# Kernel optimization log

Hardware: AMD Instinct MI355X
Metric: run time of the kernel (lower is better)

Reference implementation:

```python
import jax, jax.numpy as jnp
import numpy as np

N = 32768       # total nodes across the batch of graphs
E = 524288      # total edges
D = 512         # feature dim (dimensions = [512, 512, 512])
G = 512         # number of graphs (64 nodes each)


def setup_inputs() -> dict:
    key = jax.random.key(0)
    ks = jax.random.split(key, 16)
    inp = {
        'feat': jax.random.normal(ks[0], (N, D), jnp.float32),
        'src': jax.random.randint(ks[1], (E,), 0, N, jnp.int32),
        'dst': jax.random.randint(ks[2], (E,), 0, N, jnp.int32),
        'adj_vals': jax.random.uniform(ks[3], (E,), jnp.float32),
        'graph_ids': (jnp.arange(N, dtype=jnp.int32) // (N // G)),
        'W0': jax.random.normal(ks[4], (D, D), jnp.float32) * 0.05,
        'b0': jnp.zeros((D,), jnp.float32),
        'W1': jax.random.normal(ks[5], (D, D), jnp.float32) * 0.05,
        'b1': jnp.zeros((D,), jnp.float32),
        'gW1': jax.random.normal(ks[6], (D, D), jnp.float32) * 0.05,
        'gb1': jnp.zeros((D,), jnp.float32),
        'gW2': jax.random.normal(ks[7], (D, D), jnp.float32) * 0.05,
        'gb2': jnp.zeros((D,), jnp.float32),
        'gW3': jax.random.normal(ks[8], (D, D), jnp.float32) * 0.05,
        'gb3': jnp.zeros((D,), jnp.float32),
        'gWs': jax.random.normal(ks[9], (D, D), jnp.float32) * 0.05,
        'gbs': jnp.zeros((D,), jnp.float32),
    }
    return inp


def reference(feat, src, dst, adj_vals, graph_ids,
              W0, b0, W1, b1,
              gW1, gb1, gW2, gb2, gW3, gb3, gWs, gbs):
    # GCN layer: act(A_hat @ (X W) + b), A_hat given as weighted edge list
    def gcn(h, W, b, act):
        support = h @ W                              # [N, D]
        msg = adj_vals[:, None] * support[src]       # [E, D]
        agg = jax.ops.segment_sum(msg, dst, num_segments=N)
        return act(agg + b)

    h = gcn(feat, W0, b0, jax.nn.relu)               # hidden layer, act=relu
    h = gcn(h, W1, b1, lambda x: x)                  # last layer, identity act

    # pooling: per-graph mean readout -> sigmoid -> repeat-expand back to nodes
    ones = jnp.ones((N, 1), h.dtype)
    counts = jax.ops.segment_sum(ones, graph_ids, num_segments=G)   # [G, 1]
    pooled = jax.ops.segment_sum(h, graph_ids, num_segments=G) / counts
    g = jax.nn.sigmoid(pooled)[graph_ids]            # [N, D] repeat-expanded

    z = jax.nn.relu(g @ gW1 + gb1)
    z = jax.nn.relu(z @ gW2 + gb2)
    z = jax.nn.relu(z @ gW3 + gb3)
    return z + (g @ gWs + gbs)
```

## Files before the change

kernel.cpp:

```cpp
#include <hip/hip_runtime.h>

typedef unsigned int u32;
typedef unsigned short u16;

typedef __attribute__((ext_vector_type(8))) __bf16 bf16x8;
typedef __attribute__((ext_vector_type(4))) float f32x4;
typedef __attribute__((ext_vector_type(2))) float f32x2;
typedef __attribute__((ext_vector_type(4))) u32 u32x4;

#define N_NODES 32768
#define N_EDGES 524288
#define DIM 512
#define N_GRAPHS 512
#define ECAP_ROW 768
#define ECAP 1216
#define ELDS_SZ (ECAP + ECAP / 32 + 1)
#define NB_CONV 8192
#define NB_TR 1536

__device__ __forceinline__ u16 f2b(float f) {
  union { float f; u32 u; } v; v.f = f;
  u32 r = v.u + 0x7FFFu + ((v.u >> 16) & 1u);
  return (u16)(r >> 16);
}
__device__ __forceinline__ u32 pack2(float a, float b) {
  return (u32)f2b(a) | ((u32)f2b(b) << 16);
}
__device__ __forceinline__ float blo(u32 u) { union { u32 u; float f; } v; v.u = u << 16; return v.f; }
__device__ __forceinline__ float bhi(u32 u) { union { u32 u; float f; } v; v.u = u & 0xFFFF0000u; return v.f; }
__device__ __forceinline__ float b2f(u16 u) { union { u32 u; float f; } v; v.u = ((u32)u) << 16; return v.f; }

__device__ __forceinline__ void async16(const void* g, void* l) {
  __builtin_amdgcn_global_load_lds(
      (const __attribute__((address_space(1))) u32*)g,
      (__attribute__((address_space(3))) u32*)l, 16, 0, 0);
}

__device__ __forceinline__ int eidx(int i) { return i + (i >> 5); }

__device__ __forceinline__ void acc8(f32x2* a, u32x4 raw, float v) {
  f32x2 v2 = {v, v};
  a[0] += v2 * f32x2{blo(raw.x), bhi(raw.x)};
  a[1] += v2 * f32x2{blo(raw.y), bhi(raw.y)};
  a[2] += v2 * f32x2{blo(raw.z), bhi(raw.z)};
  a[3] += v2 * f32x2{blo(raw.w), bhi(raw.w)};
}

struct WPack {
  const float* src[6];
  u16* dst[6];
};
__global__ __launch_bounds__(256)
void k_prep(const float* __restrict__ feat, u16* __restrict__ featb, WPack wp,
            const int* __restrict__ dstv, int* __restrict__ counts) {
  __shared__ float tile[32][33];
  const int bid = blockIdx.x, tid = threadIdx.x;
  if (bid < NB_CONV) {
    int i = bid * 256 + tid;
    const float4* p = (const float4*)feat;
    float4 a = p[2 * i], b = p[2 * i + 1];
    uint4 o;
    o.x = pack2(a.x, a.y); o.y = pack2(a.z, a.w);
    o.z = pack2(b.x, b.y); o.w = pack2(b.z, b.w);
    ((uint4*)featb)[i] = o;
  } else if (bid < NB_CONV + NB_TR) {
    int idx = bid - NB_CONV;
    int bz = idx >> 8, rem = idx & 255, by = rem >> 4, bx = rem & 15;
    const float* W = wp.src[bz];
    u16* Wt = wp.dst[bz];
    int tx = tid & 31, ty = tid >> 5;
    int bx32 = bx * 32, by32 = by * 32;
    #pragma unroll
    for (int i = 0; i < 4; i++)
      tile[ty + 8 * i][tx] = W[(size_t)(by32 + ty + 8 * i) * DIM + bx32 + tx];
    __syncthreads();
    #pragma unroll
    for (int i = 0; i < 4; i++)
      Wt[(size_t)(bx32 + ty + 8 * i) * DIM + by32 + tx] = f2b(tile[tx][ty + 8 * i]);
  } else {
    int i = (bid - NB_CONV - NB_TR) * 256 + tid;
    atomicAdd(&counts[dstv[i]], 1);
  }
}

__global__ void k_scan(const int* __restrict__ counts, int* __restrict__ offsets,
                       int* __restrict__ cursor) {
  __shared__ int part[1024];
  int t = threadIdx.x;
  const int4* c4 = (const int4*)counts;
  int4 cv[8];
  #pragma unroll
  for (int j = 0; j < 8; j++) cv[j] = c4[t * 8 + j];
  int loc[32];
  int s = 0;
  #pragma unroll
  for (int j = 0; j < 8; j++) {
    loc[4 * j + 0] = s; s += cv[j].x;
    loc[4 * j + 1] = s; s += cv[j].y;
    loc[4 * j + 2] = s; s += cv[j].z;
    loc[4 * j + 3] = s; s += cv[j].w;
  }
  part[t] = s;
  __syncthreads();
  for (int off = 1; off < 1024; off <<= 1) {
    int v = (t >= off) ? part[t - off] : 0;
    __syncthreads();
    part[t] += v;
    __syncthreads();
  }
  int excl = (t == 0) ? 0 : part[t - 1];
  #pragma unroll
  for (int j = 0; j < 8; j++) {
    int4 o = make_int4(excl + loc[4 * j], excl + loc[4 * j + 1],
                       excl + loc[4 * j + 2], excl + loc[4 * j + 3]);
    ((int4*)offsets)[t * 8 + j] = o;
    ((int4*)cursor)[t * 8 + j] = o;
  }
  if (t == 1023) offsets[N_NODES] = excl + s;
}

__global__ void k_fill(const int* __restrict__ src, const int* __restrict__ dst,
                       const float* __restrict__ vals, int* __restrict__ cursor,
                       int2* __restrict__ epack) {
  int i = blockIdx.x * 256 + threadIdx.x;
  if (i >= N_EDGES) return;
  int d = dst[i];
  int p = atomicAdd(&cursor[d], 1);
  epack[p] = make_int2(src[i] | ((d & 63) << 15), __float_as_int(vals[i]));
}

__global__ __launch_bounds__(256)
void k_gemm_bt(const u16* __restrict__ A, const u16* __restrict__ Bt,
               u16* __restrict__ Cout, int M, int Nout, int K) {
  __shared__ __align__(16) u16 As[128 * 32];
  __shared__ __align__(16) u16 Bs[128 * 32];
  const int tid = threadIdx.x;
  const int l = tid & 63;
  const int w = tid >> 6;
  const int mBase = blockIdx.x * 128;
  const int nBase = blockIdx.y * 128;
  const int wm = (w >> 1) * 64;
  const int wn = (w & 1) * 64;
  const int lrow = l >> 2;
  const int lcol = (l & 3) * 8;
  const int q = l >> 4;
  const int r = l & 15;
  f32x4 acc[4][4] = {};

  for (int k0 = 0; k0 < K; k0 += 32) {
    #pragma unroll
    for (int p = 0; p < 2; p++) {
      int row = w * 32 + p * 16 + lrow;
      async16(A + (size_t)(mBase + row) * K + k0 + lcol, (char*)As + w * 2048 + p * 1024);
      async16(Bt + (size_t)(nBase + row) * K + k0 + lcol, (char*)Bs + w * 2048 + p * 1024);
    }
    __syncthreads();
    bf16x8 af[4], bfr[4];
    #pragma unroll
    for (int i = 0; i < 4; i++) af[i] = *(const bf16x8*)&As[(wm + i * 16 + r) * 32 + q * 8];
    #pragma unroll
    for (int j = 0; j < 4; j++) bfr[j] = *(const bf16x8*)&Bs[(wn + j * 16 + r) * 32 + q * 8];
    #pragma unroll
    for (int i = 0; i < 4; i++)
      #pragma unroll
      for (int j = 0; j < 4; j++)
        acc[i][j] = __builtin_amdgcn_mfma_f32_16x16x32_bf16(af[i], bfr[j], acc[i][j], 0, 0, 0);
    __syncthreads();
  }

  #pragma unroll
  for (int i = 0; i < 4; i++) {
    #pragma unroll
    for (int j = 0; j < 4; j++) {
      int col = nBase + wn + j * 16 + r;
      #pragma unroll
      for (int reg = 0; reg < 4; reg++) {
        int rowg = mBase + wm + i * 16 + q * 4 + reg;
        Cout[(size_t)rowg * Nout + col] = f2b(acc[i][j][reg]);
      }
    }
  }
}

template <bool RELU, bool ADDEND, bool OUTF32, bool SIGMOID>
__global__ __launch_bounds__(256)
void k_gemm_small(const u16* __restrict__ A, const u16* __restrict__ Bt,
                  const float* __restrict__ bias, const u16* __restrict__ addend,
                  void* __restrict__ Cout, int Nout, int K) {
  __shared__ __align__(16) u16 As[64 * 32];
  __shared__ __align__(16) u16 Bs[64 * 32];
  const int tid = threadIdx.x;
  const int l = tid & 63;
  const int w = tid >> 6;
  const int mBase = blockIdx.x * 64;
  const int nBase = blockIdx.y * 64;
  const int wm = (w >> 1) * 32;
  const int wn = (w & 1) * 32;
  const int lrow = tid >> 2;
  const int lcol = (tid & 3) * 8;
  const int q = l >> 4;
  const int r = l & 15;
  f32x4 acc[2][2] = {};

  for (int k0 = 0; k0 < K; k0 += 32) {
    async16(A + (size_t)(mBase + lrow) * K + k0 + lcol, (char*)As + tid * 16);
    async16(Bt + (size_t)(nBase + lrow) * K + k0 + lcol, (char*)Bs + tid * 16);
    __syncthreads();
    bf16x8 af[2], bfr[2];
    #pragma unroll
    for (int i = 0; i < 2; i++) af[i] = *(const bf16x8*)&As[(wm + i * 16 + r) * 32 + q * 8];
    #pragma unroll
    for (int j = 0; j < 2; j++) bfr[j] = *(const bf16x8*)&Bs[(wn + j * 16 + r) * 32 + q * 8];
    #pragma unroll
    for (int i = 0; i < 2; i++)
      #pragma unroll
      for (int j = 0; j < 2; j++)
        acc[i][j] = __builtin_amdgcn_mfma_f32_16x16x32_bf16(af[i], bfr[j], acc[i][j], 0, 0, 0);
    __syncthreads();
  }

  #pragma unroll
  for (int i = 0; i < 2; i++) {
    #pragma unroll
    for (int j = 0; j < 2; j++) {
      int col = nBase + wn + j * 16 + r;
      float bv = bias[col];
      #pragma unroll
      for (int reg = 0; reg < 4; reg++) {
        int rowg = mBase + wm + i * 16 + q * 4 + reg;
        float v = acc[i][j][reg] + bv;
        if (ADDEND) v += b2f(addend[(size_t)rowg * Nout + col]);
        if (RELU) v = fmaxf(v, 0.0f);
        if (SIGMOID) v = 1.0f / (1.0f + expf(-v));
        if (OUTF32) ((float*)Cout)[(size_t)rowg * Nout + col] = v;
        else ((u16*)Cout)[(size_t)rowg * Nout + col] = f2b(v);
      }
    }
  }
}

__global__ __launch_bounds__(256)
void k_agg_row(const u16* __restrict__ support, const int* __restrict__ offsets,
               const int2* __restrict__ epack, const float* __restrict__ bias,
               u16* __restrict__ outp) {
  __shared__ int2 eLds[ECAP_ROW];
  __shared__ unsigned char permLds[32];
  const int tid = threadIdx.x;
  const int chunk = blockIdx.x & 7;
  const int gidx  = blockIdx.x >> 3;
  const int rowBase = gidx * 32;
  const int e0b = offsets[rowBase];
  const int nb = offsets[rowBase + 32] - e0b;
  const bool fits = (nb <= ECAP_ROW);

  if (tid < 32) {
    int deg = offsets[rowBase + tid + 1] - offsets[rowBase + tid];
    u32 key = ((u32)deg << 8) | (u32)tid;
    #pragma unroll
    for (int k = 2; k <= 32; k <<= 1) {
      #pragma unroll
      for (int j = k >> 1; j >= 1; j >>= 1) {
        u32 o = __shfl_xor(key, j);
        bool lower = (tid & j) == 0;
        bool asc = (tid & k) == 0;
        key = ((key < o) == (lower == asc)) ? key : o;
      }
    }
    permLds[tid] = (unsigned char)(key & 255u);
  }
  if (fits) {
    for (int i = tid; i < nb; i += 256) eLds[i] = epack[e0b + i];
  }
  __syncthreads();

  const int wi = tid >> 6;
  const int l  = tid & 63;
  const int grp = l >> 3;
  const int li  = l & 7;
  const int colOff = chunk * 64 + li * 8;
  const u16* spc = support + colOff;

  const int rl = permLds[wi * 8 + grp];
  const int r = rowBase + rl;
  const int re0 = offsets[r] - e0b;
  const int deg = offsets[r + 1] - e0b - re0;

  f32x2 a[4];
  {
    const float4* bp = (const float4*)(bias + colOff);
    float4 x = bp[0], y = bp[1];
    a[0] = f32x2{x.x, x.y}; a[1] = f32x2{x.z, x.w};
    a[2] = f32x2{y.x, y.y}; a[3] = f32x2{y.z, y.w};
  }

  if (fits) {
    int i = 0;
    for (; i + 8 <= deg; i += 8) {
      int2 p[8];
      #pragma unroll
      for (int j = 0; j < 8; j++) p[j] = eLds[re0 + i + j];
      u32x4 rw[8];
      #pragma unroll
      for (int j = 0; j < 8; j++)
        rw[j] = *(const u32x4*)(spc + (size_t)(p[j].x & 32767) * DIM);
      #pragma unroll
      for (int j = 0; j < 8; j++) acc8(a, rw[j], __int_as_float(p[j].y));
    }
    for (; i < deg; i++) {
      int2 p = eLds[re0 + i];
      u32x4 rw = *(const u32x4*)(spc + (size_t)(p.x & 32767) * DIM);
      acc8(a, rw, __int_as_float(p.y));
    }
  } else {
    for (int i = 0; i < deg; i++) {
      int2 p = epack[e0b + re0 + i];
      u32x4 rw = *(const u32x4*)(spc + (size_t)(p.x & 32767) * DIM);
      acc8(a, rw, __int_as_float(p.y));
    }
  }

  #pragma unroll
  for (int i = 0; i < 4; i++) {
    a[i].x = fmaxf(a[i].x, 0.0f);
    a[i].y = fmaxf(a[i].y, 0.0f);
  }
  u32x4 o;
  o.x = pack2(a[0].x, a[0].y); o.y = pack2(a[1].x, a[1].y);
  o.z = pack2(a[2].x, a[2].y); o.w = pack2(a[3].x, a[3].y);
  *(u32x4*)(outp + (size_t)r * DIM + colOff) = o;
}

__global__ __launch_bounds__(256)
void k_agg_pool(const u16* __restrict__ support, const int* __restrict__ offsets,
                const int2* __restrict__ epack, u16* __restrict__ outp) {
  __shared__ int2 eLds[ELDS_SZ];
  __shared__ float redLds[256];

  const int tid = threadIdx.x;
  const int chunk = blockIdx.x & 7;
  const int cidx = blockIdx.x >> 3;
  const int rowBase = cidx * 64;
  const int e0b = offsets[rowBase];
  const int nb = offsets[rowBase + 64] - e0b;
  const bool fits = (nb <= ECAP);

  if (fits) {
    for (int i = tid; i < nb; i += 256) eLds[eidx(i)] = epack[e0b + i];
  }
  __syncthreads();

  const int slot = tid >> 3;
  const int li = tid & 7;
  const int colOff = chunk * 64 + li * 8;
  const u16* spc = support + colOff;
  const int e0 = (nb * slot) >> 5;
  const int e1 = (nb * (slot + 1)) >> 5;

  f32x2 psum[4] = {};

  auto consume = [&](int2 p, u32x4 rw) {
    float v = __int_as_float(p.y);
    f32x2 v2 = {v, v};
    psum[0] += v2 * f32x2{blo(rw.x), bhi(rw.x)};
    psum[1] += v2 * f32x2{blo(rw.y), bhi(rw.y)};
    psum[2] += v2 * f32x2{blo(rw.z), bhi(rw.z)};
    psum[3] += v2 * f32x2{blo(rw.w), bhi(rw.w)};
  };

  if (fits) {
    int i = e0;
    for (; i + 8 <= e1; i += 8) {
      int2 p[8];
      #pragma unroll
      for (int j = 0; j < 8; j++) p[j] = eLds[eidx(i + j)];
      u32x4 rw[8];
      #pragma unroll
      for (int j = 0; j < 8; j++)
        rw[j] = *(const u32x4*)(spc + (size_t)(p[j].x & 32767) * DIM);
      #pragma unroll
      for (int j = 0; j < 8; j++) consume(p[j], rw[j]);
    }
    for (; i < e1; i++) {
      int2 p = eLds[eidx(i)];
      u32x4 rw = *(const u32x4*)(spc + (size_t)(p.x & 32767) * DIM);
      consume(p, rw);
    }
  } else {
    for (int i = e0; i < e1; i++) {
      int2 p = epack[e0b + i];
      u32x4 rw = *(const u32x4*)(spc + (size_t)(p.x & 32767) * DIM);
      consume(p, rw);
    }
  }

  #pragma unroll
  for (int k = 0; k < 4; k++) {
    psum[k].x += __shfl_xor(psum[k].x, 8);  psum[k].y += __shfl_xor(psum[k].y, 8);
    psum[k].x += __shfl_xor(psum[k].x, 16); psum[k].y += __shfl_xor(psum[k].y, 16);
    psum[k].x += __shfl_xor(psum[k].x, 32); psum[k].y += __shfl_xor(psum[k].y, 32);
  }
  const int wi = tid >> 6;
  if (((tid >> 3) & 7) == 0) {
    #pragma unroll
    for (int k = 0; k < 4; k++) {
      redLds[wi * 64 + li * 8 + 2 * k]     = psum[k].x;
      redLds[wi * 64 + li * 8 + 2 * k + 1] = psum[k].y;
    }
  }
  __syncthreads();
  if (tid < 64) {
    float s = redLds[tid] + redLds[64 + tid] + redLds[128 + tid] + redLds[192 + tid];
    outp[(size_t)cidx * DIM + chunk * 64 + tid] = f2b(s * (1.0f / 64.0f));
  }
}

__global__ void k_expand(const float* __restrict__ small, float* __restrict__ out) {
  int i = blockIdx.x * 256 + threadIdx.x;
  int col4 = i & 127;
  int node = i >> 7;
  float4 v = ((const float4*)small)[((node >> 6) << 7) + col4];
  ((float4*)out)[i] = v;
}

extern "C" void kernel_launch(void* const* d_in, const int* in_sizes, int n_in,
                              void* d_out, int out_size, void* d_ws, size_t ws_size,
                              hipStream_t stream) {
  const float* feat = (const float*)d_in[0];
  const int* src    = (const int*)d_in[1];
  const int* dst    = (const int*)d_in[2];
  const float* adj  = (const float*)d_in[3];
  const float* W0  = (const float*)d_in[5];
  const float* b0  = (const float*)d_in[6];
  const float* W1  = (const float*)d_in[7];
  const float* b1  = (const float*)d_in[8];
  const float* gW1 = (const float*)d_in[9];
  const float* gb1 = (const float*)d_in[10];
  const float* gW2 = (const float*)d_in[11];
  const float* gb2 = (const float*)d_in[12];
  const float* gW3 = (const float*)d_in[13];
  const float* gb3 = (const float*)d_in[14];
  const float* gWs = (const float*)d_in[15];
  const float* gbs = (const float*)d_in[16];

  char* ws = (char*)d_ws;
  size_t off = 0;
  auto alloc = [&](size_t bytes) -> void* {
    void* p = ws + off;
    off = (off + bytes + 255) & ~(size_t)255;
    return p;
  };
  u16* bufA = (u16*)alloc((size_t)N_NODES * DIM * 2);
  u16* bufB = (u16*)alloc((size_t)N_NODES * DIM * 2);
  u16* wt[6];
  for (int i = 0; i < 6; i++) wt[i] = (u16*)alloc((size_t)DIM * DIM * 2);
  int* counts   = (int*)alloc((size_t)N_NODES * 4);
  int* offsets  = (int*)alloc((size_t)(N_NODES + 1) * 4);
  int* cursor   = (int*)alloc((size_t)N_NODES * 4);
  int2* epack   = (int2*)alloc((size_t)N_EDGES * 8);
  u16* qb       = (u16*)alloc((size_t)N_GRAPHS * DIM * 2);
  u16* gfeat    = (u16*)alloc((size_t)N_GRAPHS * DIM * 2);
  u16* z1       = (u16*)alloc((size_t)N_GRAPHS * DIM * 2);
  u16* z2       = (u16*)alloc((size_t)N_GRAPHS * DIM * 2);
  u16* z3       = (u16*)alloc((size_t)N_GRAPHS * DIM * 2);
  float* osmall = (float*)alloc((size_t)N_GRAPHS * DIM * 4);

  (void)hipMemsetAsync(counts, 0, (size_t)N_NODES * 4, stream);

  WPack wp;
  wp.src[0] = W0; wp.src[1] = W1; wp.src[2] = gW1; wp.src[3] = gW2; wp.src[4] = gW3; wp.src[5] = gWs;
  for (int i = 0; i < 6; i++) wp.dst[i] = wt[i];

  k_prep<<<NB_CONV + NB_TR + N_EDGES / 256, 256, 0, stream>>>(feat, bufA, wp, dst, counts);
  k_scan<<<1, 1024, 0, stream>>>(counts, offsets, cursor);
  k_fill<<<N_EDGES / 256, 256, 0, stream>>>(src, dst, adj, cursor, epack);

  k_gemm_bt<<<dim3(N_NODES / 128, DIM / 128), 256, 0, stream>>>(bufA, wt[0], bufB, N_NODES, DIM, DIM);
  k_agg_row<<<8192, 256, 0, stream>>>(bufB, offsets, epack, b0, bufA);
  k_agg_pool<<<4096, 256, 0, stream>>>(bufA, offsets, epack, qb);
  k_gemm_small<false, false, false, true><<<dim3(8, 8), 256, 0, stream>>>(qb, wt[1], b1, nullptr, gfeat, DIM, DIM);

  k_gemm_small<true, false, false, false><<<dim3(8, 8), 256, 0, stream>>>(gfeat, wt[2], gb1, nullptr, z1, DIM, DIM);
  k_gemm_small<true, false, false, false><<<dim3(8, 8), 256, 0, stream>>>(z1, wt[3], gb2, nullptr, z2, DIM, DIM);
  k_gemm_small<true, false, false, false><<<dim3(8, 8), 256, 0, stream>>>(z2, wt[4], gb3, nullptr, z3, DIM, DIM);
  k_gemm_small<false, true, true, false><<<dim3(8, 8), 256, 0, stream>>>(gfeat, wt[5], gbs, z3, osmall, DIM, DIM);

  k_expand<<<(N_NODES * DIM / 4) / 256, 256, 0, stream>>>(osmall, (float*)d_out);
}
```

Before: 383.9 us.

## Fuse the five small per-graph GEMMs into one LDS-resident kernel

```diff
diff --git a/kernel.cpp b/kernel.cpp
--- a/kernel.cpp
+++ b/kernel.cpp
@@ -17,6 +17,7 @@
 #define ELDS_SZ (ECAP + ECAP / 32 + 1)
 #define NB_CONV 8192
 #define NB_TR 1536
+#define FFP 520
 
 __device__ __forceinline__ u16 f2b(float f) {
   union { float f; u32 u; } v; v.f = f;
@@ -182,59 +183,87 @@
   }
 }
 
-template <bool RELU, bool ADDEND, bool OUTF32, bool SIGMOID>
-__global__ __launch_bounds__(256)
-void k_gemm_small(const u16* __restrict__ A, const u16* __restrict__ Bt,
-                  const float* __restrict__ bias, const u16* __restrict__ addend,
-                  void* __restrict__ Cout, int Nout, int K) {
-  __shared__ __align__(16) u16 As[64 * 32];
-  __shared__ __align__(16) u16 Bs[64 * 32];
+template <int ACT>
+__device__ __forceinline__ void ff_stage(const u16* Ain, const u16* __restrict__ Wt,
+                                         const float* __restrict__ bias, u16* Aout,
+                                         int l, int wv) {
+  const int r15 = l & 15;
+  const int q = l >> 4;
+  #pragma unroll
+  for (int t = 0; t < 4; t++) {
+    const int ct = wv * 4 + t;
+    f32x4 acc = {};
+    #pragma unroll
+    for (int k0 = 0; k0 < 512; k0 += 32) {
+      bf16x8 af = *(const bf16x8*)&Ain[r15 * FFP + k0 + q * 8];
+      bf16x8 bf = *(const bf16x8*)&Wt[(size_t)(ct * 16 + r15) * 512 + k0 + q * 8];
+      acc = __builtin_amdgcn_mfma_f32_16x16x32_bf16(af, bf, acc, 0, 0, 0);
+    }
+    const int c = ct * 16 + r15;
+    const float bv = bias[c];
+    #pragma unroll
+    for (int reg = 0; reg < 4; reg++) {
+      float v = acc[reg] + bv;
+      v = ACT ? fmaxf(v, 0.0f) : (1.0f / (1.0f + expf(-v)));
+      Aout[(q * 4 + reg) * FFP + c] = f2b(v);
+    }
+  }
+}
+
+__global__ __launch_bounds__(512)
+void k_ff(const u16* __restrict__ qb,
+          const u16* __restrict__ w1, const float* __restrict__ b1,
+          const u16* __restrict__ w2, const float* __restrict__ gb1,
+          const u16* __restrict__ w3, const float* __restrict__ gb2,
+          const u16* __restrict__ w4, const float* __restrict__ gb3,
+          const u16* __restrict__ w5, const float* __restrict__ gbs,
+          float* __restrict__ osmall) {
+  __shared__ __align__(16) u16 G[16 * FFP];
+  __shared__ __align__(16) u16 Z0[16 * FFP];
+  __shared__ __align__(16) u16 Z1[16 * FFP];
   const int tid = threadIdx.x;
   const int l = tid & 63;
-  const int w = tid >> 6;
-  const int mBase = blockIdx.x * 64;
-  const int nBase = blockIdx.y * 64;
-  const int wm = (w >> 1) * 32;
-  const int wn = (w & 1) * 32;
-  const int lrow = tid >> 2;
-  const int lcol = (tid & 3) * 8;
+  const int wv = tid >> 6;
+  const int rBase = blockIdx.x * 16;
+
+  for (int i = tid; i < 16 * 64; i += 512) {
+    int row = i >> 6, c8 = (i & 63) * 8;
+    *(bf16x8*)&Z0[row * FFP + c8] = *(const bf16x8*)&qb[(size_t)(rBase + row) * 512 + c8];
+  }
+  __syncthreads();
+
+  ff_stage<0>(Z0, w1, b1, G, l, wv);
+  __syncthreads();
+  ff_stage<1>(G, w2, gb1, Z0, l, wv);
+  __syncthreads();
+  ff_stage<1>(Z0, w3, gb2, Z1, l, wv);
+  __syncthreads();
+  ff_stage<1>(Z1, w4, gb3, Z0, l, wv);
+  __syncthreads();
+
+  {
+    const int r15 = l & 15;
+    const int q = l >> 6 ? 0 : l >> 4;
+  }
+  const int r15 = l & 15;
   const int q = l >> 4;
-  const int r = l & 15;
-  f32x4 acc[2][2] = {};
-
-  for (int k0 = 0; k0 < K; k0 += 32) {
-    async16(A + (size_t)(mBase + lrow) * K + k0 + lcol, (char*)As + tid * 16);
-    async16(Bt + (size_t)(nBase + lrow) * K + k0 + lcol, (char*)Bs + tid * 16);
-    __syncthreads();
-    bf16x8 af[2], bfr[2];
-    #pragma unroll
-    for (int i = 0; i < 2; i++) af[i] = *(const bf16x8*)&As[(wm + i * 16 + r) * 32 + q * 8];
-    #pragma unroll
-    for (int j = 0; j < 2; j++) bfr[j] = *(const bf16x8*)&Bs[(wn + j * 16 + r) * 32 + q * 8];
-    #pragma unroll
-    for (int i = 0; i < 2; i++)
-      #pragma unroll
-      for (int j = 0; j < 2; j++)
-        acc[i][j] = __builtin_amdgcn_mfma_f32_16x16x32_bf16(af[i], bfr[j], acc[i][j], 0, 0, 0);
-    __syncthreads();
-  }
-
-  #pragma unroll
-  for (int i = 0; i < 2; i++) {
-    #pragma unroll
-    for (int j = 0; j < 2; j++) {
-      int col = nBase + wn + j * 16 + r;
-      float bv = bias[col];
-      #pragma unroll
-      for (int reg = 0; reg < 4; reg++) {
-        int rowg = mBase + wm + i * 16 + q * 4 + reg;
-        float v = acc[i][j][reg] + bv;
-        if (ADDEND) v += b2f(addend[(size_t)rowg * Nout + col]);
-        if (RELU) v = fmaxf(v, 0.0f);
-        if (SIGMOID) v = 1.0f / (1.0f + expf(-v));
-        if (OUTF32) ((float*)Cout)[(size_t)rowg * Nout + col] = v;
-        else ((u16*)Cout)[(size_t)rowg * Nout + col] = f2b(v);
-      }
+  #pragma unroll
+  for (int t = 0; t < 4; t++) {
+    const int ct = wv * 4 + t;
+    f32x4 acc = {};
+    #pragma unroll
+    for (int k0 = 0; k0 < 512; k0 += 32) {
+      bf16x8 af = *(const bf16x8*)&G[r15 * FFP + k0 + q * 8];
+      bf16x8 bf = *(const bf16x8*)&w5[(size_t)(ct * 16 + r15) * 512 + k0 + q * 8];
+      acc = __builtin_amdgcn_mfma_f32_16x16x32_bf16(af, bf, acc, 0, 0, 0);
+    }
+    const int c = ct * 16 + r15;
+    const float bv = gbs[c];
+    #pragma unroll
+    for (int reg = 0; reg < 4; reg++) {
+      int row = q * 4 + reg;
+      float v = acc[reg] + bv + b2f(Z0[row * FFP + c]);
+      osmall[(size_t)(rBase + row) * 512 + c] = v;
     }
   }
 }
@@ -458,10 +487,6 @@
   int* cursor   = (int*)alloc((size_t)N_NODES * 4);
   int2* epack   = (int2*)alloc((size_t)N_EDGES * 8);
   u16* qb       = (u16*)alloc((size_t)N_GRAPHS * DIM * 2);
-  u16* gfeat    = (u16*)alloc((size_t)N_GRAPHS * DIM * 2);
-  u16* z1       = (u16*)alloc((size_t)N_GRAPHS * DIM * 2);
-  u16* z2       = (u16*)alloc((size_t)N_GRAPHS * DIM * 2);
-  u16* z3       = (u16*)alloc((size_t)N_GRAPHS * DIM * 2);
   float* osmall = (float*)alloc((size_t)N_GRAPHS * DIM * 4);
 
   (void)hipMemsetAsync(counts, 0, (size_t)N_NODES * 4, stream);
@@ -477,12 +502,9 @@
   k_gemm_bt<<<dim3(N_NODES / 128, DIM / 128), 256, 0, stream>>>(bufA, wt[0], bufB, N_NODES, DIM, DIM);
   k_agg_row<<<8192, 256, 0, stream>>>(bufB, offsets, epack, b0, bufA);
   k_agg_pool<<<4096, 256, 0, stream>>>(bufA, offsets, epack, qb);
-  k_gemm_small<false, false, false, true><<<dim3(8, 8), 256, 0, stream>>>(qb, wt[1], b1, nullptr, gfeat, DIM, DIM);
-
-  k_gemm_small<true, false, false, false><<<dim3(8, 8), 256, 0, stream>>>(gfeat, wt[2], gb1, nullptr, z1, DIM, DIM);
-  k_gemm_small<true, false, false, false><<<dim3(8, 8), 256, 0, stream>>>(z1, wt[3], gb2, nullptr, z2, DIM, DIM);
-  k_gemm_small<true, false, false, false><<<dim3(8, 8), 256, 0, stream>>>(z2, wt[4], gb3, nullptr, z3, DIM, DIM);
-  k_gemm_small<false, true, true, false><<<dim3(8, 8), 256, 0, stream>>>(gfeat, wt[5], gbs, z3, osmall, DIM, DIM);
+
+  k_ff<<<32, 512, 0, stream>>>(qb, wt[1], b1, wt[2], gb1, wt[3], gb2,
+                               wt[4], gb3, wt[5], gbs, osmall);
 
   k_expand<<<(N_NODES * DIM / 4) / 256, 256, 0, stream>>>(osmall, (float*)d_out);
 }
```

Result: slower. 420.1 us (+9.4%).
